# Kernel optimization log

Hardware: AMD Instinct MI355X
Metric: run time of the kernel (lower is better)

## Reference

```python
import jax, jax.numpy as jnp
import numpy as np

ALPHA = 0.2  # LeakyReLU negative slope
NEG_INF = -9e15


def setup_inputs() -> dict:
    key = jax.random.key(0)
    k1, k2, k3, k4, k5 = jax.random.split(key, 5)
    B, N, D = 4, 4096, 256
    feat = jax.random.normal(k1, (B, N, D), dtype=jnp.float32)
    adj = jax.random.randint(k2, (B, N, N), 0, 2, dtype=jnp.int32)
    W = jax.random.normal(k3, (D, D), dtype=jnp.float32) * (1.414 / np.sqrt(D))
    a_1 = jax.random.normal(k4, (D, 1), dtype=jnp.float32) * 0.1
    a_2 = jax.random.normal(k5, (D, 1), dtype=jnp.float32) * 0.1
    return {"feat": feat, "adj": adj, "W": W, "a_1": a_1, "a_2": a_2}


def reference(feat, adj, W, a_1, a_2):
    # h: [B, N, D]
    h = jnp.matmul(feat, W)
    Ax = jnp.matmul(h, a_1)  # [B, N, 1]
    Ay = jnp.matmul(h, a_2)  # [B, N, 1]
    # logits[b, i, j] = Ax[b, j] + Ay[b, i]
    logits = jnp.swapaxes(Ax, 1, 2) + Ay  # [B, N, N]
    e = jax.nn.leaky_relu(logits, negative_slope=ALPHA)
    e = jnp.where(adj > 0, e, jnp.float32(NEG_INF))
    attention = jax.nn.softmax(e, axis=-1)  # dropout p=0.0 -> identity
    h_prime = jnp.matmul(attention, feat)  # [B, N, in_features]
    h_out = jnp.matmul(h_prime, W)  # [B, N, out_features]
    return jax.nn.elu(h_out)
```

## Files before the change

### kernel.cpp

```cpp
#include <hip/hip_runtime.h>

typedef __attribute__((ext_vector_type(8))) short short8;
typedef __attribute__((ext_vector_type(4))) float f32x4;
typedef __attribute__((ext_vector_type(4))) int i32x4;
typedef __attribute__((ext_vector_type(2))) unsigned u32x2;

#define LOG2E 1.44269504f

__device__ __forceinline__ short f2bf(float f) {
  unsigned u = __builtin_bit_cast(unsigned, f);
  u += 0x7fffu + ((u >> 16) & 1u);
  return (short)(u >> 16);
}

__global__ void gat_wvec(const float* __restrict__ W, const float* __restrict__ a1,
                         const float* __restrict__ a2, float* __restrict__ w1,
                         float* __restrict__ w2) {
  __shared__ float a1f[256], a2f[256];
  const int tid = threadIdx.x;
  a1f[tid] = a1[tid];
  a2f[tid] = a2[tid];
  __syncthreads();
  float s1 = 0.f, s2 = 0.f;
  const float4* wr = (const float4*)(W + (size_t)tid * 256);
  for (int d0 = 0; d0 < 64; ++d0) {
    float4 v = wr[d0];
    s1 += v.x * a1f[d0 * 4] + v.y * a1f[d0 * 4 + 1] + v.z * a1f[d0 * 4 + 2] + v.w * a1f[d0 * 4 + 3];
    s2 += v.x * a2f[d0 * 4] + v.y * a2f[d0 * 4 + 1] + v.z * a2f[d0 * 4 + 2] + v.w * a2f[d0 * 4 + 3];
  }
  w1[tid] = s1;
  w2[tid] = s2;
}

__global__ void packB(const float* __restrict__ src, short* __restrict__ dst, int F) {
  const int tid = threadIdx.x;
  const int f = blockIdx.x, b = blockIdx.y;
  const int g = tid >> 4, l15 = tid & 15;
  const float* s = src + ((size_t)b * F * 32 + f * 32) * 256 + g * 16 + l15;
  short* d = dst + (((size_t)(b * F + f) * 16 + g) * 64) * 8;
#pragma unroll
  for (int q = 0; q < 4; ++q) {
    short8 v;
#pragma unroll
    for (int j8 = 0; j8 < 8; ++j8) v[j8] = f2bf(s[(q * 8 + j8) * 256]);
    *(short8*)(d + (q * 16 + l15) * 8) = v;
  }
}

__global__ void gat_axay(const float* __restrict__ feat, const float* __restrict__ w1,
                         const float* __restrict__ w2, float* __restrict__ AxL,
                         float* __restrict__ AyL) {
  const int lane = threadIdx.x & 63;
  const int row = blockIdx.x * 4 + (threadIdx.x >> 6);
  float4 fv = *(const float4*)(feat + (size_t)row * 256 + lane * 4);
  const float4 w1v = *(const float4*)(w1 + lane * 4);
  const float4 w2v = *(const float4*)(w2 + lane * 4);
  float s1 = fv.x * w1v.x + fv.y * w1v.y + fv.z * w1v.z + fv.w * w1v.w;
  float s2 = fv.x * w2v.x + fv.y * w2v.y + fv.z * w2v.z + fv.w * w2v.w;
#pragma unroll
  for (int off = 32; off >= 1; off >>= 1) {
    s1 += __shfl_xor(s1, off);
    s2 += __shfl_xor(s2, off);
  }
  if (lane == 0) { AxL[row] = s1 * LOG2E; AyL[row] = s2 * LOG2E; }
}

__global__ void gat_max(const float* __restrict__ AxL, float* __restrict__ MbL) {
  __shared__ float red[256];
  const int b = blockIdx.x, tid = threadIdx.x;
  float m = -3.4e38f;
  for (int i = tid; i < 4096; i += 256) m = fmaxf(m, AxL[b * 4096 + i]);
  red[tid] = m;
  __syncthreads();
  for (int s = 128; s > 0; s >>= 1) {
    if (tid < s) red[tid] = fmaxf(red[tid], red[tid + s]);
    __syncthreads();
  }
  if (tid == 0) MbL[b] = red[0];
}

__global__ __launch_bounds__(512, 4) void gat_attn(
    const short* __restrict__ featB,
    const int* __restrict__ adj,
    const float* __restrict__ AxL, const float* __restrict__ AyL,
    const float* __restrict__ MbL,
    const short* __restrict__ WB,
    float* __restrict__ out)
{
  __shared__ short smem[16896];

  const int tid = threadIdx.x;
  const int blk = blockIdx.x;
  const int x = blk & 7;
  const int b = x >> 1;
  const int it = ((blk >> 3) << 1) | (x & 1);
  const int i0 = it << 5;
  const int scoff = (blk >> 3) & 15;

  const int lane = tid & 63;
  const int aw = tid >> 6;

  float aLk[4], ddk[4];
#pragma unroll
  for (int k = 0; k < 4; ++k) {
    float ayL = AyL[b * 4096 + i0 + aw * 4 + k];
    float sL = ayL + MbL[b];
    float mrL = fmaxf(sL, 0.2f * sL);
    aLk[k] = ayL - mrL;
    ddk[k] = -0.8f * mrL;
  }
  const int* adjr = adj + ((size_t)(b * 4096 + i0 + aw * 4)) * 4096 + lane * 4;
  const float4* axp = (const float4*)(AxL + b * 4096) + lane;

  const int w = aw;
  const int rowg = (w & 1) << 4;
  const int cgrp = (w >> 1) << 2;
  const int l15 = lane & 15;
  const int q = lane >> 4;

  f32x4 acc[4], lac;
  lac = (f32x4){0.f, 0.f, 0.f, 0.f};
#pragma unroll
  for (int j = 0; j < 4; ++j) acc[j] = (f32x4){0.f, 0.f, 0.f, 0.f};

  short8 ones;
#pragma unroll
  for (int j = 0; j < 8; ++j) ones[j] = (short)0x3F80;

  const short* fbb = featB + (size_t)b * 128 * 16 * 64 * 8 + lane * 8;

  i32x4 adv[4];
  float4 axv;
  {
    const int w0 = scoff;
#pragma unroll
    for (int k = 0; k < 4; ++k)
      adv[k] = __builtin_nontemporal_load((const i32x4*)(adjr) + k * 1024 + w0 * 64);
    axv = axp[w0 * 64];
  }

  for (int sc = 0; sc < 16; ++sc) {
    const int wsc = (scoff + sc) & 15;
    const int pb = (sc & 1) * 8448;
    {
      const float* af = (const float*)&axv;
#pragma unroll
      for (int k = 0; k < 4; ++k) {
        unsigned pr[4];
#pragma unroll
        for (int u = 0; u < 4; ++u) {
          float v = af[u] + aLk[k];
          float uu = fmaxf(v, fmaf(0.2f, v, ddk[k]));
          unsigned ub = adv[k][u] > 0 ? __builtin_bit_cast(unsigned, uu) : 0xFF800000u;
          float p = __builtin_amdgcn_exp2f(__builtin_bit_cast(float, ub));
          pr[u] = __builtin_bit_cast(unsigned, p) + 0x8000u;
        }
        u32x2 pw;
        pw[0] = __builtin_amdgcn_perm(pr[1], pr[0], 0x07060302u);
        pw[1] = __builtin_amdgcn_perm(pr[3], pr[2], 0x07060302u);
        *(u32x2*)(smem + pb + (aw * 4 + k) * 264 + lane * 4) = pw;
      }
    }
    __syncthreads();

    if (sc < 15) {
      const int wn = (scoff + sc + 1) & 15;
#pragma unroll
      for (int k = 0; k < 4; ++k)
        adv[k] = __builtin_nontemporal_load((const i32x4*)(adjr) + k * 1024 + wn * 64);
      axv = axp[wn * 64];
    }

#pragma unroll
    for (int h = 0; h < 8; ++h) {
      const int f = wsc * 8 + h;
      const short* fb = fbb + (((size_t)f * 16 + cgrp) << 9);
      short8 a = *(const short8*)(smem + pb + (rowg + l15) * 264 + h * 32 + q * 8);
      lac = __builtin_amdgcn_mfma_f32_16x16x32_bf16(a, ones, lac, 0, 0, 0);
#pragma unroll
      for (int ct = 0; ct < 4; ++ct) {
        short8 bf = *(const short8*)(fb + (ct << 9));
        acc[ct] = __builtin_amdgcn_mfma_f32_16x16x32_bf16(a, bf, acc[ct], 0, 0, 0);
      }
    }
  }

  float linv[4];
#pragma unroll
  for (int reg = 0; reg < 4; ++reg) {
    float l = lac[reg];
    linv[reg] = l > 0.f ? 1.f / l : 0.f;
  }

  __syncthreads();
  short* hbuf = smem;
#pragma unroll
  for (int reg = 0; reg < 4; ++reg) {
    const int lr = rowg + q * 4 + reg;
#pragma unroll
    for (int ct = 0; ct < 4; ++ct)
      hbuf[lr * 264 + cgrp * 16 + ct * 16 + l15] = f2bf(acc[ct][reg] * linv[reg]);
  }
  __syncthreads();

  f32x4 ac2[4];
#pragma unroll
  for (int j = 0; j < 4; ++j) ac2[j] = (f32x4){0.f, 0.f, 0.f, 0.f};

  const short* wbb = WB + lane * 8;
#pragma unroll
  for (int f = 0; f < 8; ++f) {
    short8 a = *(const short8*)&hbuf[(rowg + l15) * 264 + f * 32 + q * 8];
    const short* wb = wbb + (((size_t)f * 16 + cgrp) << 9);
#pragma unroll
    for (int ct = 0; ct < 4; ++ct) {
      short8 bf = *(const short8*)(wb + (ct << 9));
      ac2[ct] = __builtin_amdgcn_mfma_f32_16x16x32_bf16(a, bf, ac2[ct], 0, 0, 0);
    }
  }

#pragma unroll
  for (int reg = 0; reg < 4; ++reg) {
    const int row = i0 + rowg + q * 4 + reg;
    float* orow = out + ((size_t)(b * 4096 + row)) * 256 + cgrp * 16 + l15;
#pragma unroll
    for (int ct = 0; ct < 4; ++ct) {
      float v = ac2[ct][reg];
      float o = v > 0.f ? v : (__builtin_amdgcn_exp2f(v * LOG2E) - 1.f);
      __builtin_nontemporal_store(o, orow + ct * 16);
    }
  }
}

extern "C" void kernel_launch(void* const* d_in, const int* in_sizes, int n_in,
                              void* d_out, int out_size, void* d_ws, size_t ws_size,
                              hipStream_t stream) {
  (void)in_sizes; (void)n_in; (void)out_size; (void)ws_size;
  const float* feat = (const float*)d_in[0];
  const int* adj = (const int*)d_in[1];
  const float* W = (const float*)d_in[2];
  const float* a1 = (const float*)d_in[3];
  const float* a2 = (const float*)d_in[4];
  float* out = (float*)d_out;

  char* ws = (char*)d_ws;
  short* featB   = (short*)ws;
  short* WB      = (short*)(ws + 8388608);
  float* AxL     = (float*)(ws + 8519680);
  float* AyL     = (float*)(ws + 8585216);
  float* MbL     = (float*)(ws + 8650752);
  float* w1      = (float*)(ws + 8651776);
  float* w2      = (float*)(ws + 8652800);

  hipLaunchKernelGGL(gat_wvec, dim3(1), dim3(256), 0, stream, W, a1, a2, w1, w2);
  hipLaunchKernelGGL(packB, dim3(8, 1), dim3(256), 0, stream, W, WB, 8);
  hipLaunchKernelGGL(packB, dim3(128, 4), dim3(256), 0, stream, feat, featB, 128);
  hipLaunchKernelGGL(gat_axay, dim3(4096), dim3(256), 0, stream, feat, w1, w2, AxL, AyL);
  hipLaunchKernelGGL(gat_max, dim3(4), dim3(256), 0, stream, AxL, MbL);
  hipLaunchKernelGGL(gat_attn, dim3(512), dim3(512), 0, stream, featB, adj, AxL, AyL, MbL, WB, out);
}
```

Before: 446.1 us.

## Pre-pack adjacency into bitmasks before attention kernel

Adds a streaming kernel that turns the int32 adjacency matrix into 64-bit ballot bitmasks, one bit per edge. The attention kernel then loads a few uniform 64-bit words per row chunk and tests its lane's bit, instead of issuing large per-lane int4 loads of adjacency inside the main loop. This takes heavy, latency-bound global loads out of the softmax/MFMA loop. In exchange it adds an extra kernel that still reads all of adjacency once and writes an 8 MB mask, which may cost about as much as the traffic it removes.

```diff
diff --git a/kernel.cpp b/kernel.cpp
--- a/kernel.cpp
+++ b/kernel.cpp
@@ -79,9 +79,25 @@
   if (tid == 0) MbL[b] = red[0];
 }
 
+__global__ void gat_pack(const int* __restrict__ adj, unsigned long long* __restrict__ bmk) {
+  const int tid = threadIdx.x;
+  const int lane = tid & 63;
+  const size_t W = ((size_t)blockIdx.x * 256 + tid) >> 6;
+  i32x4 v = __builtin_nontemporal_load((const i32x4*)(adj + W * 256) + lane);
+  unsigned long long b0 = __ballot(v[0] > 0);
+  unsigned long long b1 = __ballot(v[1] > 0);
+  unsigned long long b2 = __ballot(v[2] > 0);
+  unsigned long long b3 = __ballot(v[3] > 0);
+  if (lane < 4) {
+    unsigned long long w01 = (lane & 1) ? b1 : b0;
+    unsigned long long w23 = (lane & 1) ? b3 : b2;
+    bmk[W * 4 + lane] = (lane & 2) ? w23 : w01;
+  }
+}
+
 __global__ __launch_bounds__(512, 4) void gat_attn(
     const short* __restrict__ featB,
-    const int* __restrict__ adj,
+    const unsigned long long* __restrict__ bmk,
     const float* __restrict__ AxL, const float* __restrict__ AyL,
     const float* __restrict__ MbL,
     const short* __restrict__ WB,
@@ -109,7 +125,7 @@
     aLk[k] = ayL - mrL;
     ddk[k] = -0.8f * mrL;
   }
-  const int* adjr = adj + ((size_t)(b * 4096 + i0 + aw * 4)) * 4096 + lane * 4;
+  const unsigned long long* bmr = bmk + ((size_t)(b * 4096 + i0 + aw * 4)) * 64;
   const float4* axp = (const float4*)(AxL + b * 4096) + lane;
 
   const int w = aw;
@@ -129,13 +145,14 @@
 
   const short* fbb = featB + (size_t)b * 128 * 16 * 64 * 8 + lane * 8;
 
-  i32x4 adv[4];
+  unsigned long long wk[4][4];
   float4 axv;
   {
     const int w0 = scoff;
 #pragma unroll
     for (int k = 0; k < 4; ++k)
-      adv[k] = __builtin_nontemporal_load((const i32x4*)(adjr) + k * 1024 + w0 * 64);
+#pragma unroll
+      for (int u = 0; u < 4; ++u) wk[k][u] = bmr[k * 64 + w0 * 4 + u];
     axv = axp[w0 * 64];
   }
 
@@ -151,7 +168,8 @@
         for (int u = 0; u < 4; ++u) {
           float v = af[u] + aLk[k];
           float uu = fmaxf(v, fmaf(0.2f, v, ddk[k]));
-          unsigned ub = adv[k][u] > 0 ? __builtin_bit_cast(unsigned, uu) : 0xFF800000u;
+          unsigned keep = (unsigned)(wk[k][u] >> lane) & 1u;
+          unsigned ub = keep ? __builtin_bit_cast(unsigned, uu) : 0xFF800000u;
           float p = __builtin_amdgcn_exp2f(__builtin_bit_cast(float, ub));
           pr[u] = __builtin_bit_cast(unsigned, p) + 0x8000u;
         }
@@ -167,7 +185,8 @@
       const int wn = (scoff + sc + 1) & 15;
 #pragma unroll
       for (int k = 0; k < 4; ++k)
-        adv[k] = __builtin_nontemporal_load((const i32x4*)(adjr) + k * 1024 + wn * 64);
+#pragma unroll
+        for (int u = 0; u < 4; ++u) wk[k][u] = bmr[k * 64 + wn * 4 + u];
       axv = axp[wn * 64];
     }
 
@@ -244,18 +263,20 @@
   float* out = (float*)d_out;
 
   char* ws = (char*)d_ws;
-  short* featB   = (short*)ws;
-  short* WB      = (short*)(ws + 8388608);
-  float* AxL     = (float*)(ws + 8519680);
-  float* AyL     = (float*)(ws + 8585216);
-  float* MbL     = (float*)(ws + 8650752);
-  float* w1      = (float*)(ws + 8651776);
-  float* w2      = (float*)(ws + 8652800);
-
+  short* featB = (short*)ws;
+  unsigned long long* bmk = (unsigned long long*)(ws + 8388608);
+  short* WB    = (short*)(ws + 16777216);
+  float* AxL   = (float*)(ws + 16908288);
+  float* AyL   = (float*)(ws + 16973824);
+  float* MbL   = (float*)(ws + 17039360);
+  float* w1    = (float*)(ws + 17040384);
+  float* w2    = (float*)(ws + 17041408);
+
+  hipLaunchKernelGGL(gat_pack, dim3(65536), dim3(256), 0, stream, adj, bmk);
   hipLaunchKernelGGL(gat_wvec, dim3(1), dim3(256), 0, stream, W, a1, a2, w1, w2);
   hipLaunchKernelGGL(packB, dim3(8, 1), dim3(256), 0, stream, W, WB, 8);
   hipLaunchKernelGGL(packB, dim3(128, 4), dim3(256), 0, stream, feat, featB, 128);
   hipLaunchKernelGGL(gat_axay, dim3(4096), dim3(256), 0, stream, feat, w1, w2, AxL, AyL);
   hipLaunchKernelGGL(gat_max, dim3(4), dim3(256), 0, stream, AxL, MbL);
-  hipLaunchKernelGGL(gat_attn, dim3(512), dim3(512), 0, stream, featB, adj, AxL, AyL, MbL, WB, out);
-}
+  hipLaunchKernelGGL(gat_attn, dim3(512), dim3(512), 0, stream, featB, bmk, AxL, AyL, MbL, WB, out);
+}
```

Result: slower. 470.2 us (+5.4%).
